# Kernel optimization log

Measured on AMD Instinct MI355X. Metric: run time of the kernel, lower is better.

Reference implementation:

```python
import jax, jax.numpy as jnp
import numpy as np

N_EMBD = 2048
N_HEAD = 16
N_KV_HEAD = 4
HEAD_DIM = N_EMBD // N_HEAD  # 128
N_REP = N_HEAD // N_KV_HEAD  # 4
ROPE_BASE = 1000000.0
B, T = 2, 2048


def _rotate_half(x):
    x1, x2 = jnp.split(x, 2, axis=-1)
    return jnp.concatenate([-x2, x1], axis=-1)


def _rope(q, k, t):
    # q: [b,t,h,d], k: [b,t,kvh,d]; full rotary (partial_rotary_factor=1.0)
    pos = jnp.arange(t, dtype=jnp.float32)
    inv_freq = 1.0 / (ROPE_BASE ** (jnp.arange(0, HEAD_DIM, 2, dtype=jnp.float32) / HEAD_DIM))
    ang = pos[:, None] * inv_freq[None, :]                      # [t, d/2]
    cos = jnp.concatenate([jnp.cos(ang), jnp.cos(ang)], -1)     # [t, d]
    sin = jnp.concatenate([jnp.sin(ang), jnp.sin(ang)], -1)
    cos = cos[None, :, None, :]
    sin = sin[None, :, None, :]
    q = q * cos + _rotate_half(q) * sin
    k = k * cos + _rotate_half(k) * sin
    return q, k


def setup_inputs() -> dict:
    key = jax.random.key(0)
    ks = jax.random.split(key, 9)
    std = 0.02
    proj_std = 0.02 / np.sqrt(2 * 24)
    return {
        "x": jax.random.normal(ks[0], (B, T, N_EMBD), dtype=jnp.float32),
        "Wq": jax.random.normal(ks[1], (N_EMBD, N_HEAD * HEAD_DIM), dtype=jnp.float32) * std,
        "bq": jnp.zeros((N_HEAD * HEAD_DIM,), dtype=jnp.float32),
        "Wk": jax.random.normal(ks[2], (N_EMBD, N_KV_HEAD * HEAD_DIM), dtype=jnp.float32) * std,
        "bk": jnp.zeros((N_KV_HEAD * HEAD_DIM,), dtype=jnp.float32),
        "Wv": jax.random.normal(ks[3], (N_EMBD, N_KV_HEAD * HEAD_DIM), dtype=jnp.float32) * std,
        "bv": jnp.zeros((N_KV_HEAD * HEAD_DIM,), dtype=jnp.float32),
        "Wo": jax.random.normal(ks[4], (N_EMBD, N_EMBD), dtype=jnp.float32) * proj_std,
        "bo": jnp.zeros((N_EMBD,), dtype=jnp.float32),
    }


def reference(x, Wq, bq, Wk, bk, Wv, bv, Wo, bo):
    b, t, _ = x.shape
    q = (x @ Wq + bq).reshape(b, t, N_HEAD, HEAD_DIM)
    k = (x @ Wk + bk).reshape(b, t, N_KV_HEAD, HEAD_DIM)
    v = (x @ Wv + bv).reshape(b, t, N_KV_HEAD, HEAD_DIM)
    q, k = _rope(q, k, t)
    # repeat_kv: expand kv heads by n_rep
    k = jnp.broadcast_to(k[:, :, :, None, :], (b, t, N_KV_HEAD, N_REP, HEAD_DIM)).reshape(b, t, N_HEAD, HEAD_DIM)
    v = jnp.broadcast_to(v[:, :, :, None, :], (b, t, N_KV_HEAD, N_REP, HEAD_DIM)).reshape(b, t, N_HEAD, HEAD_DIM)
    qh = q.transpose(0, 2, 1, 3)  # [b,h,t,d]
    kh = k.transpose(0, 2, 1, 3)
    vh = v.transpose(0, 2, 1, 3)
    causal = jnp.tril(jnp.ones((t, t), dtype=bool))[None, None]  # [1,1,t,t]
    bias = jnp.where(causal, 0.0, -1e9).astype(jnp.float32)
    scores = jnp.einsum('bhtd,bhTd->bhtT', qh, kh) / jnp.sqrt(jnp.float32(HEAD_DIM))
    attn_w = jax.nn.softmax(scores + bias, axis=-1)
    attn_out = jnp.einsum('bhtT,bhTd->bhtd', attn_w, vh)
    attn = attn_out.transpose(0, 2, 1, 3).reshape(b, t, N_EMBD)
    return attn @ Wo + bo
```

## Files before the change

### kernel.cpp

```cpp
#include <hip/hip_runtime.h>

typedef _Float16 f16x8 __attribute__((ext_vector_type(8)));
typedef _Float16 f16x4 __attribute__((ext_vector_type(4)));
typedef float    f32x4 __attribute__((ext_vector_type(4)));

__device__ __forceinline__ void gload16(const void* g, void* l) {
  __builtin_amdgcn_global_load_lds((const __attribute__((address_space(1))) void*)g,
                                   (__attribute__((address_space(3))) void*)l, 16, 0, 0);
}

__global__ __launch_bounds__(256) void cast_f32_f16(const float* __restrict__ src,
                                                    _Float16* __restrict__ dst, int n4) {
  int i = blockIdx.x * 256 + threadIdx.x;
  if (i < n4) {
    f32x4 v = *(const f32x4*)(src + (size_t)i * 4);
    f16x4 o;
    o[0] = (_Float16)v[0]; o[1] = (_Float16)v[1];
    o[2] = (_Float16)v[2]; o[3] = (_Float16)v[3];
    *(f16x4*)(dst + (size_t)i * 4) = o;
  }
}

__global__ __launch_bounds__(256) void wqkvtrans_kernel(const float* __restrict__ Wq,
                                                        const float* __restrict__ Wk,
                                                        const float* __restrict__ Wv,
                                                        _Float16* __restrict__ dst) {
  const int n0 = blockIdx.x * 64, k0 = blockIdx.y * 64;
  const float* src; int N, nb;
  if (n0 < 2048)      { src = Wq; N = 2048; nb = n0; }
  else if (n0 < 2560) { src = Wk; N = 512;  nb = n0 - 2048; }
  else                { src = Wv; N = 512;  nb = n0 - 2560; }
  __shared__ float tile[64][65];
#pragma unroll
  for (int i = 0; i < 16; ++i) {
    int id = i * 256 + threadIdx.x;
    int kk = id >> 6, nn = id & 63;
    tile[kk][nn] = src[(size_t)(k0 + kk) * N + nb + nn];
  }
  __syncthreads();
#pragma unroll
  for (int i = 0; i < 16; ++i) {
    int id = i * 256 + threadIdx.x;
    int nn = id >> 6, kk = id & 63;
    dst[(size_t)(n0 + nn) * 2048 + k0 + kk] = (_Float16)tile[kk][nn];
  }
}

__global__ __launch_bounds__(256) void wtrans_kernel(const float* __restrict__ src,
                                                     _Float16* __restrict__ dst,
                                                     int N, int K, int rowOff, int ldDst) {
  const int n0 = blockIdx.x * 64, k0 = blockIdx.y * 64;
  __shared__ float tile[64][65];
#pragma unroll
  for (int i = 0; i < 16; ++i) {
    int id = i * 256 + threadIdx.x;
    int kk = id >> 6, nn = id & 63;
    tile[kk][nn] = src[(size_t)(k0 + kk) * N + n0 + nn];
  }
  __syncthreads();
#pragma unroll
  for (int i = 0; i < 16; ++i) {
    int id = i * 256 + threadIdx.x;
    int nn = id >> 6, kk = id & 63;
    dst[(size_t)(rowOff + n0 + nn) * ldDst + k0 + kk] = (_Float16)tile[kk][nn];
  }
}

__global__ __launch_bounds__(256) void biaspack_kernel(const float* __restrict__ bq,
                                                       const float* __restrict__ bk,
                                                       const float* __restrict__ bv,
                                                       float* __restrict__ out) {
  int i = blockIdx.x * 256 + threadIdx.x;
  if (i < 3072) out[i] = (i < 2048) ? bq[i] : (i < 2560 ? bk[i - 2048] : bv[i - 2560]);
}

template <bool F16OUT>
__global__ __launch_bounds__(256) void gemm_nt(const _Float16* __restrict__ A,
                                               const _Float16* __restrict__ B,
                                               const float* __restrict__ bias,
                                               void* __restrict__ Cv,
                                               int M, int N, int K) {
  __shared__ __align__(16) _Float16 As[128][64];
  __shared__ __align__(16) _Float16 Bs[128][64];
  const int tid = threadIdx.x;
  const int lane = tid & 63, wave = tid >> 6;
  const int wr = wave >> 1, wc = wave & 1;
  const int r = lane & 15, g = lane >> 4;
  const int rb = blockIdx.y * 128, cb = blockIdx.x * 128;

  const int swz = ((tid & 7) ^ ((tid >> 3) & 7)) * 8;
  const _Float16* aSrc = A + (size_t)(rb + (tid >> 3)) * K + swz;
  const _Float16* bSrc = B + (size_t)(cb + (tid >> 3)) * K + swz;

  f32x4 acc[4][4] = {};

  for (int kt = 0; kt < K; kt += 64) {
    __syncthreads();
#pragma unroll
    for (int p = 0; p < 4; ++p) {
      gload16(aSrc + (size_t)(p * 32) * K + kt, (_Float16*)As + (p * 256 + wave * 64) * 8);
      gload16(bSrc + (size_t)(p * 32) * K + kt, (_Float16*)Bs + (p * 256 + wave * 64) * 8);
    }
    __syncthreads();
#pragma unroll
    for (int kk = 0; kk < 2; ++kk) {
      f16x8 af[4], bf[4];
#pragma unroll
      for (int m = 0; m < 4; ++m) {
        int row = wr * 64 + m * 16 + r;
        af[m] = *(const f16x8*)(&As[row][((kk * 4 + g) ^ (row & 7)) * 8]);
      }
#pragma unroll
      for (int n = 0; n < 4; ++n) {
        int row = wc * 64 + n * 16 + r;
        bf[n] = *(const f16x8*)(&Bs[row][((kk * 4 + g) ^ (row & 7)) * 8]);
      }
#pragma unroll
      for (int m = 0; m < 4; ++m)
#pragma unroll
        for (int n = 0; n < 4; ++n)
          acc[m][n] = __builtin_amdgcn_mfma_f32_16x16x32_f16(af[m], bf[n], acc[m][n], 0, 0, 0);
    }
  }

  float bvals[4];
#pragma unroll
  for (int n = 0; n < 4; ++n) bvals[n] = bias[cb + wc * 64 + n * 16 + r];
#pragma unroll
  for (int m = 0; m < 4; ++m) {
#pragma unroll
    for (int n = 0; n < 4; ++n) {
#pragma unroll
      for (int j = 0; j < 4; ++j) {
        int row = rb + wr * 64 + m * 16 + g * 4 + j;
        int col = cb + wc * 64 + n * 16 + r;
        float v = acc[m][n][j] + bvals[n];
        if (F16OUT)
          ((_Float16*)Cv)[(size_t)row * N + col] = (_Float16)v;
        else
          ((float*)Cv)[(size_t)row * N + col] = v;
      }
    }
  }
}

__global__ __launch_bounds__(256) void rope_kernel(_Float16* __restrict__ QKV) {
  const int tok = blockIdx.x;
  const int t = tok & 2047;
  __shared__ float cs[64], sn[64];
  if (threadIdx.x < 64) {
    int j = threadIdx.x;
    float freq = exp2f((float)(-2 * j) * (19.931568569324174f / 128.0f));
    float ang = (float)t * freq;
    cs[j] = cosf(ang);
    sn[j] = sinf(ang);
  }
  __syncthreads();
  _Float16* base = QKV + (size_t)tok * 3072;
  int idx = threadIdx.x;
  if (idx < 160) {
    int head = idx >> 3, j0 = (idx & 7) * 8;
    int cb = (head < 16) ? head * 128 : 2048 + (head - 16) * 128;
    _Float16* p = base + cb;
    f16x8 a = *(const f16x8*)(p + j0);
    f16x8 b2 = *(const f16x8*)(p + 64 + j0);
    f16x8 oa, ob;
#pragma unroll
    for (int e = 0; e < 8; ++e) {
      float c = cs[j0 + e], s = sn[j0 + e];
      float x1 = (float)a[e], x2 = (float)b2[e];
      oa[e] = (_Float16)(x1 * c - x2 * s);
      ob[e] = (_Float16)(x2 * c + x1 * s);
    }
    *(f16x8*)(p + j0) = oa;
    *(f16x8*)(p + 64 + j0) = ob;
  }
}

__global__ __launch_bounds__(256) void vtrans_kernel(const _Float16* __restrict__ QKV,
                                                     _Float16* __restrict__ Vt) {
  const int bk = blockIdx.z;
  const int t0 = blockIdx.x * 64, d0 = blockIdx.y * 64;
  const int b = bk >> 2, kvh = bk & 3;
  __shared__ _Float16 tile[64][65];
  const _Float16* src = QKV + (size_t)b * 2048 * 3072 + 2560 + kvh * 128;
#pragma unroll
  for (int i = 0; i < 16; ++i) {
    int id = i * 256 + threadIdx.x;
    int tt = id >> 6, dd = id & 63;
    tile[tt][dd] = src[(size_t)(t0 + tt) * 3072 + d0 + dd];
  }
  __syncthreads();
  _Float16* dst = Vt + (size_t)bk * 128 * 2048;
#pragma unroll
  for (int i = 0; i < 16; ++i) {
    int id = i * 256 + threadIdx.x;
    int dd = id >> 6, tt = id & 63;
    dst[(size_t)(d0 + dd) * 2048 + t0 + tt] = tile[tt][dd];
  }
}

__global__ __launch_bounds__(512) void attn_kernel(const _Float16* __restrict__ QKV,
                                                   const _Float16* __restrict__ Vt,
                                                   _Float16* __restrict__ O) {
  const int bid = blockIdx.x;
  const int b = bid >> 8;
  const int ii = bid & 255;
  const int h = ii >> 4;
  const int qtr = ii & 15;
  const int qt = b ? 15 - qtr : qtr;
  const int tid = threadIdx.x;
  const int wave = tid >> 6, lane = tid & 63;
  const int r = lane & 15, g = lane >> 4;
  const int q0 = qt * 128 + wave * 16;
  const int kvh = h >> 2;
  const _Float16* Qb  = QKV + (size_t)b * 2048 * 3072 + h * 128;
  const _Float16* Kb  = QKV + (size_t)b * 2048 * 3072 + 2048 + kvh * 128;
  const _Float16* Vtg = Vt + (size_t)(b * 4 + kvh) * 128 * 2048;

  __shared__ __align__(16) _Float16 Klds[128][128];
  __shared__ __align__(16) _Float16 Vlds[128][128];
  __shared__ __align__(16) _Float16 Plds[8][16][64];

  const int sRow = tid >> 4;
  const int sChunk = ((tid & 15) ^ ((tid >> 4) & 7)) * 8;
  const _Float16* kSrc = Kb  + (size_t)sRow * 3072 + sChunk;
  const _Float16* vSrc = Vtg + (size_t)sRow * 2048 + sChunk;

  f16x8 qf[4];
  {
    const float qsc = 0.08838834764831845f * 1.4426950408889634f;
    const _Float16* qrow = Qb + (size_t)(q0 + r) * 3072 + g * 8;
#pragma unroll
    for (int c = 0; c < 4; ++c) {
      f16x8 v = *(const f16x8*)(qrow + c * 32);
#pragma unroll
      for (int i = 0; i < 8; ++i) v[i] = (_Float16)((float)v[i] * qsc);
      qf[c] = v;
    }
  }

  f32x4 oacc[8] = {};
  float mrun = -1e30f, lrun = 0.f;
  const int kend = qt * 128 + 128;
  const int qlim = q0 + 16;

  for (int kb = 0; kb < kend; kb += 128) {
#pragma unroll
    for (int p = 0; p < 4; ++p) {
      gload16(kSrc + (size_t)(kb + p * 32) * 3072, (_Float16*)Klds + (p * 512 + tid) * 8);
      gload16(vSrc + (size_t)(p * 32) * 2048 + kb, (_Float16*)Vlds + (p * 512 + tid) * 8);
    }
    __syncthreads();
#pragma unroll
    for (int kk2 = 0; kk2 < 128; kk2 += 64) {
      const int kbb = kb + kk2;
      if (kbb >= qlim) break;
      f32x4 sT[4] = {};
      __builtin_amdgcn_s_setprio(1);
#pragma unroll
      for (int c = 0; c < 4; ++c) {
#pragma unroll
        for (int n = 0; n < 4; ++n) {
          f16x8 kf = *(const f16x8*)(&Klds[kk2 + n * 16 + r][(((c * 4 + g) ^ (r & 7)) * 8)]);
          sT[n] = __builtin_amdgcn_mfma_f32_16x16x32_f16(kf, qf[c], sT[n], 0, 0, 0);
        }
      }
      __builtin_amdgcn_s_setprio(0);
      if (kbb + 63 > q0) {
#pragma unroll
        for (int n = 0; n < 4; ++n)
#pragma unroll
          for (int j = 0; j < 4; ++j) {
            int kg = kbb + n * 16 + g * 4 + j;
            if (kg > q0 + r) sT[n][j] = -1e30f;
          }
      }
      float mt = -1e30f;
#pragma unroll
      for (int n = 0; n < 4; ++n)
#pragma unroll
        for (int j = 0; j < 4; ++j) mt = fmaxf(mt, sT[n][j]);
      mt = fmaxf(mt, __shfl_xor(mt, 16));
      mt = fmaxf(mt, __shfl_xor(mt, 32));
      if (__any(mt > mrun)) {
        float mnew = fmaxf(mrun, mt);
        float alpha = exp2f(mrun - mnew);
        lrun *= alpha;
        float al[4];
#pragma unroll
        for (int jj = 0; jj < 4; ++jj) al[jj] = __shfl(alpha, g * 4 + jj);
#pragma unroll
        for (int dt = 0; dt < 8; ++dt)
#pragma unroll
          for (int jj = 0; jj < 4; ++jj) oacc[dt][jj] *= al[jj];
        mrun = mnew;
      }
      float p[4][4];
      float rs = 0.f;
#pragma unroll
      for (int n = 0; n < 4; ++n)
#pragma unroll
        for (int j = 0; j < 4; ++j) {
          p[n][j] = exp2f(sT[n][j] - mrun);
          rs += p[n][j];
        }
      rs += __shfl_xor(rs, 16);
      rs += __shfl_xor(rs, 32);
      lrun += rs;
      asm volatile("" ::: "memory");
#pragma unroll
      for (int n = 0; n < 4; ++n) {
        f16x4 p4;
#pragma unroll
        for (int j = 0; j < 4; ++j) p4[j] = (_Float16)p[n][j];
        int c16s = (2 * n + (g >> 1)) ^ (r & 7);
        *(f16x4*)(&Plds[wave][r][c16s * 8 + (g & 1) * 4]) = p4;
      }
      asm volatile("s_waitcnt lgkmcnt(0)" ::: "memory");
      __builtin_amdgcn_sched_barrier(0);
      f16x8 pa0 = *(const f16x8*)(&Plds[wave][r][((g) ^ (r & 7)) * 8]);
      f16x8 pa1 = *(const f16x8*)(&Plds[wave][r][((4 + g) ^ (r & 7)) * 8]);
      __builtin_amdgcn_s_setprio(1);
#pragma unroll
      for (int dt = 0; dt < 8; ++dt) {
        f16x8 vf0 = *(const f16x8*)(&Vlds[dt * 16 + r][((((kk2 >> 3) + g) ^ (r & 7)) * 8)]);
        oacc[dt] = __builtin_amdgcn_mfma_f32_16x16x32_f16(pa0, vf0, oacc[dt], 0, 0, 0);
        f16x8 vf1 = *(const f16x8*)(&Vlds[dt * 16 + r][((((kk2 >> 3) + 4 + g) ^ (r & 7)) * 8)]);
        oacc[dt] = __builtin_amdgcn_mfma_f32_16x16x32_f16(pa1, vf1, oacc[dt], 0, 0, 0);
      }
      __builtin_amdgcn_s_setprio(0);
    }
    __syncthreads();
  }

  float linv = 1.0f / lrun;
  float li[4];
#pragma unroll
  for (int jj = 0; jj < 4; ++jj) li[jj] = __shfl(linv, g * 4 + jj);
#pragma unroll
  for (int dt = 0; dt < 8; ++dt)
#pragma unroll
    for (int jj = 0; jj < 4; ++jj)
      O[(size_t)(b * 2048 + q0 + g * 4 + jj) * 2048 + h * 128 + dt * 16 + r] =
          (_Float16)(oacc[dt][jj] * li[jj]);
}

extern "C" void kernel_launch(void* const* d_in, const int* in_sizes, int n_in,
                              void* d_out, int out_size, void* d_ws, size_t ws_size,
                              hipStream_t stream) {
  const float* x  = (const float*)d_in[0];
  const float* Wq = (const float*)d_in[1];
  const float* bq = (const float*)d_in[2];
  const float* Wk = (const float*)d_in[3];
  const float* bk = (const float*)d_in[4];
  const float* Wv = (const float*)d_in[5];
  const float* bv = (const float*)d_in[6];
  const float* Wo = (const float*)d_in[7];
  const float* bo = (const float*)d_in[8];
  float* out = (float*)d_out;

  char* ws = (char*)d_ws;
  constexpr size_t QKV_OFF  = 0;
  constexpr size_t VT_OFF   = 25165824;
  constexpr size_t ATTN_OFF = VT_OFF + 4194304;
  constexpr size_t WT_OFF   = ATTN_OFF + 16777216;
  constexpr size_t BIAS_OFF = WT_OFF + 12582912;
  _Float16* QKV  = (_Float16*)(ws + QKV_OFF);
  _Float16* Vt   = (_Float16*)(ws + VT_OFF);
  _Float16* attn = (_Float16*)(ws + ATTN_OFF);
  _Float16* WT   = (_Float16*)(ws + WT_OFF);
  float*    bqkv = (float*)(ws + BIAS_OFF);
  _Float16* xb = (_Float16*)d_out;

  cast_f32_f16<<<8192, 256, 0, stream>>>(x, xb, (2 * 2048 * 2048) / 4);
  wqkvtrans_kernel<<<dim3(48, 32), 256, 0, stream>>>(Wq, Wk, Wv, WT);
  biaspack_kernel<<<12, 256, 0, stream>>>(bq, bk, bv, bqkv);
  gemm_nt<true><<<dim3(3072 / 128, 4096 / 128), 256, 0, stream>>>(xb, WT, bqkv, QKV, 4096, 3072, 2048);
  wtrans_kernel<<<dim3(32, 32), 256, 0, stream>>>(Wo, WT, 2048, 2048, 0, 2048);
  rope_kernel<<<4096, 256, 0, stream>>>(QKV);
  vtrans_kernel<<<dim3(32, 2, 8), 256, 0, stream>>>(QKV, Vt);
  attn_kernel<<<512, 512, 0, stream>>>(QKV, Vt, attn);
  gemm_nt<false><<<dim3(2048 / 128, 4096 / 128), 256, 0, stream>>>(attn, WT, bo, out, 4096, 2048, 2048);
}
```

Measured before the change: 214.8 us.

## Use double-buffered 8-wave GEMM and fold Q RoPE into attention

Replaces the single-buffered 128x128 GEMM with a templated 512-thread, double-buffered kernel that interleaves LDS fragment loads, next-tile global prefetch and MFMA phases with explicit barriers and priority hints. It uses 256x192 tiles for the QKV projection and 256x128 tiles for the output projection. RoPE for Q now runs inside the attention kernel's Q load, so the standalone RoPE pass only rotates K heads and computes sin/cos per element instead of through shared memory. The aim is to hide global-load latency, raise MFMA utilisation and cut one pass over Q, at the cost of more registers and fragile hand-tuned barrier scheduling.

```diff
diff --git a/kernel.cpp b/kernel.cpp
--- a/kernel.cpp
+++ b/kernel.cpp
@@ -74,107 +74,158 @@
   if (i < 3072) out[i] = (i < 2048) ? bq[i] : (i < 2560 ? bk[i - 2048] : bv[i - 2560]);
 }
 
-template <bool F16OUT>
-__global__ __launch_bounds__(256) void gemm_nt(const _Float16* __restrict__ A,
-                                               const _Float16* __restrict__ B,
-                                               const float* __restrict__ bias,
-                                               void* __restrict__ Cv,
-                                               int M, int N, int K) {
-  __shared__ __align__(16) _Float16 As[128][64];
-  __shared__ __align__(16) _Float16 Bs[128][64];
+template <int BM, int BN, int MWAVES, int NWAVES, bool F16OUT>
+__global__ __launch_bounds__(512, 2) void gemm8p_nt(const _Float16* __restrict__ A,
+                                                    const _Float16* __restrict__ B,
+                                                    const float* __restrict__ bias,
+                                                    void* __restrict__ Cv,
+                                                    int M, int N, int K) {
+  constexpr int WM = BM / MWAVES, WN = BN / NWAVES;
+  constexpr int MR = WM / 16, NR = WN / 16;
+  constexpr int MRH = MR / 2;
+  constexpr int NRH = (NR + 1) / 2, NRL = NR - NRH;
+  __shared__ __align__(16) _Float16 As[2][BM * 64];
+  __shared__ __align__(16) _Float16 Bs[2][BN * 64];
   const int tid = threadIdx.x;
   const int lane = tid & 63, wave = tid >> 6;
-  const int wr = wave >> 1, wc = wave & 1;
+  const int wr = wave / NWAVES, wc = wave % NWAVES;
   const int r = lane & 15, g = lane >> 4;
-  const int rb = blockIdx.y * 128, cb = blockIdx.x * 128;
+  const int rb = blockIdx.y * BM, cb = blockIdx.x * BN;
 
   const int swz = ((tid & 7) ^ ((tid >> 3) & 7)) * 8;
   const _Float16* aSrc = A + (size_t)(rb + (tid >> 3)) * K + swz;
   const _Float16* bSrc = B + (size_t)(cb + (tid >> 3)) * K + swz;
 
-  f32x4 acc[4][4] = {};
-
-  for (int kt = 0; kt < K; kt += 64) {
-    __syncthreads();
-#pragma unroll
-    for (int p = 0; p < 4; ++p) {
-      gload16(aSrc + (size_t)(p * 32) * K + kt, (_Float16*)As + (p * 256 + wave * 64) * 8);
-      gload16(bSrc + (size_t)(p * 32) * K + kt, (_Float16*)Bs + (p * 256 + wave * 64) * 8);
+  f32x4 acc[MR][NR] = {};
+  f16x8 af[MRH][2], bf[NR][2];
+
+  const int NT = K >> 6;
+
+#pragma unroll
+  for (int i = 0; i < BM / 64; ++i)
+    gload16(aSrc + (size_t)(i * 64) * K, As[0] + (i * 512 + tid) * 8);
+#pragma unroll
+  for (int i = 0; i < BN / 64; ++i)
+    gload16(bSrc + (size_t)(i * 64) * K, Bs[0] + (i * 512 + tid) * 8);
+  asm volatile("s_waitcnt vmcnt(0)" ::: "memory");
+  __builtin_amdgcn_s_barrier();
+
+  auto ldA = [&](_Float16* AsC, int mh) {
+#pragma unroll
+    for (int mi = 0; mi < MRH; ++mi)
+#pragma unroll
+      for (int kk = 0; kk < 2; ++kk) {
+        int row = wr * WM + (mh * MRH + mi) * 16 + r;
+        af[mi][kk] = *(const f16x8*)(AsC + row * 64 + (((kk * 4 + g) ^ (r & 7)) * 8));
+      }
+  };
+  auto ldB = [&](_Float16* BsC, int n0, int cnt) {
+#pragma unroll
+    for (int ni = 0; ni < NR; ++ni)
+      if (ni < cnt) {
+#pragma unroll
+        for (int kk = 0; kk < 2; ++kk) {
+          int row = wc * WN + (n0 + ni) * 16 + r;
+          bf[n0 + ni][kk] = *(const f16x8*)(BsC + row * 64 + (((kk * 4 + g) ^ (r & 7)) * 8));
+        }
+      }
+  };
+  auto mma = [&](int mh, int n0, int cnt) {
+    __builtin_amdgcn_s_setprio(1);
+#pragma unroll
+    for (int mi = 0; mi < MRH; ++mi)
+#pragma unroll
+      for (int ni = 0; ni < NR; ++ni)
+        if (ni < cnt) {
+#pragma unroll
+          for (int kk = 0; kk < 2; ++kk)
+            acc[mh * MRH + mi][n0 + ni] = __builtin_amdgcn_mfma_f32_16x16x32_f16(
+                af[mi][kk], bf[n0 + ni][kk], acc[mh * MRH + mi][n0 + ni], 0, 0, 0);
+        }
+    __builtin_amdgcn_s_setprio(0);
+  };
+
+  auto ktile = [&](_Float16* AsC, _Float16* BsC, _Float16* AsN, _Float16* BsN,
+                   int ktNext, bool doStage) {
+    ldA(AsC, 0);
+    ldB(BsC, 0, NRH);
+    if (doStage) {
+#pragma unroll
+      for (int i = 0; i < BM / 64; ++i)
+        gload16(aSrc + (size_t)ktNext * 64 + (size_t)(i * 64) * K, AsN + (i * 512 + tid) * 8);
     }
-    __syncthreads();
-#pragma unroll
-    for (int kk = 0; kk < 2; ++kk) {
-      f16x8 af[4], bf[4];
-#pragma unroll
-      for (int m = 0; m < 4; ++m) {
-        int row = wr * 64 + m * 16 + r;
-        af[m] = *(const f16x8*)(&As[row][((kk * 4 + g) ^ (row & 7)) * 8]);
-      }
-#pragma unroll
-      for (int n = 0; n < 4; ++n) {
-        int row = wc * 64 + n * 16 + r;
-        bf[n] = *(const f16x8*)(&Bs[row][((kk * 4 + g) ^ (row & 7)) * 8]);
-      }
-#pragma unroll
-      for (int m = 0; m < 4; ++m)
-#pragma unroll
-        for (int n = 0; n < 4; ++n)
-          acc[m][n] = __builtin_amdgcn_mfma_f32_16x16x32_f16(af[m], bf[n], acc[m][n], 0, 0, 0);
+    __builtin_amdgcn_s_barrier();
+    asm volatile("s_waitcnt lgkmcnt(0)" ::: "memory");
+    __builtin_amdgcn_sched_barrier(0);
+    mma(0, 0, NRH);
+    __builtin_amdgcn_s_barrier();
+    ldB(BsC, NRH, NRL);
+    if (doStage) {
+#pragma unroll
+      for (int i = 0; i < BN / 64; ++i)
+        gload16(bSrc + (size_t)ktNext * 64 + (size_t)(i * 64) * K, BsN + (i * 512 + tid) * 8);
     }
-  }
-
-  float bvals[4];
-#pragma unroll
-  for (int n = 0; n < 4; ++n) bvals[n] = bias[cb + wc * 64 + n * 16 + r];
-#pragma unroll
-  for (int m = 0; m < 4; ++m) {
-#pragma unroll
-    for (int n = 0; n < 4; ++n) {
+    __builtin_amdgcn_s_barrier();
+    asm volatile("s_waitcnt lgkmcnt(0)" ::: "memory");
+    __builtin_amdgcn_sched_barrier(0);
+    mma(0, NRH, NRL);
+    __builtin_amdgcn_s_barrier();
+    ldA(AsC, 1);
+    __builtin_amdgcn_s_barrier();
+    asm volatile("s_waitcnt lgkmcnt(0)" ::: "memory");
+    __builtin_amdgcn_sched_barrier(0);
+    mma(1, 0, NRH);
+    __builtin_amdgcn_s_barrier();
+    mma(1, NRH, NRL);
+    asm volatile("s_waitcnt vmcnt(0)" ::: "memory");
+    __builtin_amdgcn_s_barrier();
+  };
+
+  for (int kt = 0; kt < NT; kt += 2) {
+    ktile(As[0], Bs[0], As[1], Bs[1], kt + 1, kt + 1 < NT);
+    ktile(As[1], Bs[1], As[0], Bs[0], kt + 2, kt + 2 < NT);
+  }
+
+  float bvals[NR];
+#pragma unroll
+  for (int n = 0; n < NR; ++n) bvals[n] = bias[cb + wc * WN + n * 16 + r];
+#pragma unroll
+  for (int m = 0; m < MR; ++m)
+#pragma unroll
+    for (int n = 0; n < NR; ++n)
 #pragma unroll
       for (int j = 0; j < 4; ++j) {
-        int row = rb + wr * 64 + m * 16 + g * 4 + j;
-        int col = cb + wc * 64 + n * 16 + r;
+        int row = rb + wr * WM + m * 16 + g * 4 + j;
+        int col = cb + wc * WN + n * 16 + r;
         float v = acc[m][n][j] + bvals[n];
         if (F16OUT)
           ((_Float16*)Cv)[(size_t)row * N + col] = (_Float16)v;
         else
           ((float*)Cv)[(size_t)row * N + col] = v;
       }
-    }
-  }
-}
-
-__global__ __launch_bounds__(256) void rope_kernel(_Float16* __restrict__ QKV) {
-  const int tok = blockIdx.x;
+}
+
+__global__ __launch_bounds__(256) void ropek_kernel(_Float16* __restrict__ QKV) {
+  const int tid = threadIdx.x;
+  const int tok = blockIdx.x * 8 + (tid >> 5);
   const int t = tok & 2047;
-  __shared__ float cs[64], sn[64];
-  if (threadIdx.x < 64) {
-    int j = threadIdx.x;
-    float freq = exp2f((float)(-2 * j) * (19.931568569324174f / 128.0f));
-    float ang = (float)t * freq;
-    cs[j] = cosf(ang);
-    sn[j] = sinf(ang);
-  }
-  __syncthreads();
-  _Float16* base = QKV + (size_t)tok * 3072;
-  int idx = threadIdx.x;
-  if (idx < 160) {
-    int head = idx >> 3, j0 = (idx & 7) * 8;
-    int cb = (head < 16) ? head * 128 : 2048 + (head - 16) * 128;
-    _Float16* p = base + cb;
-    f16x8 a = *(const f16x8*)(p + j0);
-    f16x8 b2 = *(const f16x8*)(p + 64 + j0);
-    f16x8 oa, ob;
-#pragma unroll
-    for (int e = 0; e < 8; ++e) {
-      float c = cs[j0 + e], s = sn[j0 + e];
-      float x1 = (float)a[e], x2 = (float)b2[e];
-      oa[e] = (_Float16)(x1 * c - x2 * s);
-      ob[e] = (_Float16)(x2 * c + x1 * s);
-    }
-    *(f16x8*)(p + j0) = oa;
-    *(f16x8*)(p + 64 + j0) = ob;
-  }
+  const int idx = tid & 31;
+  const int head = idx >> 3, j0 = (idx & 7) * 8;
+  _Float16* p = QKV + (size_t)tok * 3072 + 2048 + head * 128;
+  f16x8 a = *(const f16x8*)(p + j0);
+  f16x8 b2 = *(const f16x8*)(p + 64 + j0);
+  f16x8 oa, ob;
+#pragma unroll
+  for (int e = 0; e < 8; ++e) {
+    float fr = exp2f((float)(j0 + e) * -0.31143075889569023f);
+    float ang = (float)t * fr;
+    float c = cosf(ang), s = sinf(ang);
+    float x1 = (float)a[e], x2 = (float)b2[e];
+    oa[e] = (_Float16)(x1 * c - x2 * s);
+    ob[e] = (_Float16)(x2 * c + x1 * s);
+  }
+  *(f16x8*)(p + j0) = oa;
+  *(f16x8*)(p + 64 + j0) = ob;
 }
 
 __global__ __launch_bounds__(256) void vtrans_kernel(const _Float16* __restrict__ QKV,
@@ -232,12 +283,20 @@
     const float qsc = 0.08838834764831845f * 1.4426950408889634f;
     const _Float16* qrow = Qb + (size_t)(q0 + r) * 3072 + g * 8;
 #pragma unroll
-    for (int c = 0; c < 4; ++c) {
-      f16x8 v = *(const f16x8*)(qrow + c * 32);
-#pragma unroll
-      for (int i = 0; i < 8; ++i) v[i] = (_Float16)((float)v[i] * qsc);
-      qf[c] = v;
-    }
+    for (int c = 0; c < 4; ++c) qf[c] = *(const f16x8*)(qrow + c * 32);
+    const float t = (float)(q0 + r);
+#pragma unroll
+    for (int c = 0; c < 2; ++c)
+#pragma unroll
+      for (int e = 0; e < 8; ++e) {
+        int j = c * 32 + g * 8 + e;
+        float fr = exp2f((float)j * -0.31143075889569023f);
+        float ang = t * fr;
+        float ca = cosf(ang), sa = sinf(ang);
+        float x1 = (float)qf[c][e] * qsc, x2 = (float)qf[c + 2][e] * qsc;
+        qf[c][e]     = (_Float16)(x1 * ca - x2 * sa);
+        qf[c + 2][e] = (_Float16)(x2 * ca + x1 * sa);
+      }
   }
 
   f32x4 oacc[8] = {};
@@ -376,10 +435,12 @@
   cast_f32_f16<<<8192, 256, 0, stream>>>(x, xb, (2 * 2048 * 2048) / 4);
   wqkvtrans_kernel<<<dim3(48, 32), 256, 0, stream>>>(Wq, Wk, Wv, WT);
   biaspack_kernel<<<12, 256, 0, stream>>>(bq, bk, bv, bqkv);
-  gemm_nt<true><<<dim3(3072 / 128, 4096 / 128), 256, 0, stream>>>(xb, WT, bqkv, QKV, 4096, 3072, 2048);
+  gemm8p_nt<256, 192, 2, 4, true>
+      <<<dim3(3072 / 192, 4096 / 256), 512, 0, stream>>>(xb, WT, bqkv, QKV, 4096, 3072, 2048);
   wtrans_kernel<<<dim3(32, 32), 256, 0, stream>>>(Wo, WT, 2048, 2048, 0, 2048);
-  rope_kernel<<<4096, 256, 0, stream>>>(QKV);
+  ropek_kernel<<<512, 256, 0, stream>>>(QKV);
   vtrans_kernel<<<dim3(32, 2, 8), 256, 0, stream>>>(QKV, Vt);
   attn_kernel<<<512, 512, 0, stream>>>(QKV, Vt, attn);
-  gemm_nt<false><<<dim3(2048 / 128, 4096 / 128), 256, 0, stream>>>(attn, WT, bo, out, 4096, 2048, 2048);
-}
+  gemm8p_nt<256, 128, 4, 2, false>
+      <<<dim3(2048 / 128, 4096 / 256), 512, 0, stream>>>(attn, WT, bo, out, 4096, 2048, 2048);
+}
```

After: 209.8 us. -2.3%, faster.
